# Kernel optimization log

Hardware: AMD Instinct MI355X
Metric: run time of the kernel (lower is better)

Reference implementation:

```python
import jax, jax.numpy as jnp
import numpy as np

N_NODES = 1_000_000
N_EDGES = 16_000_000


def setup_inputs() -> dict:
    key = jax.random.key(0)
    ks = jax.random.split(key, 12)
    x = jax.random.normal(ks[0], (N_NODES, 3), dtype=jnp.float32)
    edge_index = jax.random.randint(ks[1], (2, N_EDGES), 0, N_NODES, dtype=jnp.int64)
    # GCNConv uses Linear(in, out, bias=False) + separate post-aggregation bias
    def lin(k, fi, fo):
        return jax.random.normal(k, (fi, fo), dtype=jnp.float32) / np.sqrt(fi)
    W1 = lin(ks[2], 3, 4); b1 = jnp.zeros((4,), jnp.float32)
    W2 = lin(ks[3], 4, 4); b2 = jnp.zeros((4,), jnp.float32)
    W3 = lin(ks[4], 4, 3); b3 = jnp.zeros((3,), jnp.float32)
    Wc = lin(ks[5], 3, 5)
    bc = jax.random.normal(ks[6], (5,), dtype=jnp.float32) * 0.01
    return {"x": x, "edge_index": edge_index, "W1": W1, "b1": b1,
            "W2": W2, "b2": b2, "W3": W3, "b3": b3, "Wc": Wc, "bc": bc}


def reference(x, edge_index, W1, b1, W2, b2, W3, b3, Wc, bc):
    N = x.shape[0]
    loop = jnp.arange(N, dtype=edge_index.dtype)
    row = jnp.concatenate([edge_index[0], loop])  # source (with self-loops)
    col = jnp.concatenate([edge_index[1], loop])  # target (with self-loops)
    # symmetric GCN normalization: deg over targets incl. self-loops
    deg = jax.ops.segment_sum(jnp.ones_like(row, dtype=x.dtype), col, num_segments=N)
    dinv = jnp.where(deg > 0, jax.lax.rsqrt(deg), 0.0)
    norm = dinv[row] * dinv[col]  # [E+N]

    def gcn_conv(h, W, b):
        h = h @ W                              # [N, F_out]
        msg = norm[:, None] * h[row]           # gather + scale, [E+N, F_out]
        agg = jax.ops.segment_sum(msg, col, num_segments=N)
        return agg + b

    h = jnp.tanh(gcn_conv(x, W1, b1))
    h = jnp.tanh(gcn_conv(h, W2, b2))
    h = jnp.tanh(gcn_conv(h, W3, b3))
    out = h @ Wc + bc
    return (out, h)
```

## Files before the change

kernel.cpp:

```cpp
#include <hip/hip_runtime.h>


#define BKT_BITS 10
#define BKT_SZ   1024
#define MAXB     1024
#define TILE     8192
#define HTILE    4096
#define CHUNK    32768
#define TPC      4
#define SEGC     32
#define MAXSEG   32
#define ATHR     1024
#define RECSENT  0xFFFFFFFFu

typedef int v4i __attribute__((ext_vector_type(4)));

constexpr float XD_SCALE = 4096.0f;
constexpr float HD_SCALE = 16384.0f;
constexpr int   QBIAS    = 1 << 17;

__device__ __forceinline__ short q16(float v, float s) {
    int t = __float2int_rn(v * s);
    t = max(-32767, min(32767, t));
    return (short)t;
}

__device__ __forceinline__ unsigned blk_exscan(unsigned cnt, unsigned* woff) {
    int tid = threadIdx.x, lane = tid & 63, wid = tid >> 6;
    unsigned v = cnt;
#pragma unroll
    for (int d = 1; d < 64; d <<= 1) {
        unsigned t = __shfl_up(v, d);
        if (lane >= d) v += t;
    }
    if (lane == 63) woff[wid] = v;
    __syncthreads();
    if (tid < 16) {
        unsigned w = woff[tid];
        unsigned iw = w;
#pragma unroll
        for (int d = 1; d < 16; d <<= 1) {
            unsigned t = __shfl_up(iw, d, 16);
            if (tid >= d) iw += t;
        }
        woff[tid] = iw - w;
    }
    __syncthreads();
    return (v - cnt) + woff[wid];
}

__device__ __forceinline__ void ld_tile(const int* __restrict__ p, long t0, long t1,
                                        int tid, int4* dst, int sentinel) {
#pragma unroll
    for (int v = 0; v < 2; ++v) {
        long e = t0 + (long)v * HTILE + (long)tid * 4;
        if (e + 3 < t1) {
            dst[v] = *(const int4*)(p + e);
        } else {
            int* d = (int*)&dst[v];
#pragma unroll
            for (int j = 0; j < 4; ++j) d[j] = (e + j < t1) ? p[e + j] : sentinel;
        }
    }
}

__global__ __launch_bounds__(ATHR) void k_hist(const int* __restrict__ col, int E,
                                               unsigned short* __restrict__ cnt16) {
    __shared__ unsigned lh[MAXB];
    lh[threadIdx.x] = 0u;
    __syncthreads();
    long e0 = (long)blockIdx.x * TILE;
    long e1 = e0 + TILE; if (e1 > E) e1 = E;
    int4 c4[2];
    ld_tile(col, e0, e1, threadIdx.x, c4, -1);
#pragma unroll
    for (int v = 0; v < 2; ++v) {
        const int* cc = (const int*)&c4[v];
#pragma unroll
        for (int j = 0; j < 4; ++j) {
            unsigned b = ((unsigned)cc[j]) >> BKT_BITS;
            if (b < MAXB) atomicAdd(&lh[b], 1u);
        }
    }
    __syncthreads();
    cnt16[(size_t)blockIdx.x * MAXB + threadIdx.x] = (unsigned short)lh[threadIdx.x];
}

__global__ __launch_bounds__(256) void k_offA(const unsigned short* __restrict__ cnt16,
                                              int ntile, unsigned* __restrict__ psum) {
    int seg = blockIdx.x >> 2;
    int b = ((blockIdx.x & 3) << 8) + threadIdx.x;
    int tlo = seg * SEGC * TPC;
    int thi = (seg + 1) * SEGC * TPC; if (thi > ntile) thi = ntile;
    unsigned s = 0;
    for (int t = tlo; t < thi; ++t) s += cnt16[(size_t)t * MAXB + b];
    psum[seg * MAXB + b] = s;
}

__global__ __launch_bounds__(256) void k_totB(const unsigned* __restrict__ psum, int nseg,
                                              unsigned* __restrict__ bcnt) {
    int b = blockIdx.x * blockDim.x + threadIdx.x;
    unsigned s = 0;
    for (int g = 0; g < nseg; ++g) s += psum[g * MAXB + b];
    bcnt[b] = s;
}

__global__ __launch_bounds__(1024) void k_scan2(const unsigned* __restrict__ bcnt,
                                                unsigned* __restrict__ bpfx, int NB) {
    __shared__ unsigned tot[MAXB], pfx[MAXB];
    int b = threadIdx.x;
    tot[b] = (b < NB) ? bcnt[b] : 0u;
    __syncthreads();
    if (b == 0) {
        unsigned run = 0;
        for (int i = 0; i < MAXB; ++i) { pfx[i] = run; run += tot[i]; }
    }
    __syncthreads();
    bpfx[b] = pfx[b];
}

__global__ __launch_bounds__(1024) void k_offB(unsigned* __restrict__ psum, int nseg,
                                               const unsigned* __restrict__ bpfx) {
    int b = threadIdx.x;
    unsigned run = bpfx[b];
    for (int g = 0; g < nseg; ++g) {
        unsigned t = psum[g * MAXB + b];
        psum[g * MAXB + b] = run;
        run += t;
    }
}

__global__ __launch_bounds__(256) void k_offC(const unsigned short* __restrict__ cnt16,
                                              int ntile,
                                              const unsigned* __restrict__ psum,
                                              unsigned* __restrict__ offs, int nblk) {
    int seg = blockIdx.x >> 2;
    int b = ((blockIdx.x & 3) << 8) + threadIdx.x;
    int clo = seg * SEGC;
    int chi = clo + SEGC; if (chi > nblk) chi = nblk;
    unsigned run = psum[seg * MAXB + b];
    for (int c = clo; c < chi; ++c) {
        offs[(size_t)c * MAXB + b] = run;
        int tlo = c * TPC, thi = tlo + TPC; if (thi > ntile) thi = ntile;
        for (int t = tlo; t < thi; ++t) run += cnt16[(size_t)t * MAXB + b];
    }
}

__global__ __launch_bounds__(ATHR, 8) void k_place(const int* __restrict__ row,
                                                   const int* __restrict__ col, int E,
                                                   const unsigned* __restrict__ offs,
                                                   const unsigned short* __restrict__ cnt16,
                                                   unsigned* __restrict__ recbuf, int NB) {
    __shared__ unsigned lo[MAXB], cnt[MAXB], sc[MAXB], pc[MAXB];
    __shared__ unsigned rec[TILE];
    __shared__ unsigned short bkt[TILE];
    __shared__ unsigned woff[16];
    int tid = threadIdx.x;
    lo[tid] = (tid < NB) ? offs[(size_t)blockIdx.x * MAXB + tid] : 0u;
    long base = (long)blockIdx.x * CHUNK;
    long bend = base + CHUNK; if (bend > E) bend = E;
    int ntl = (int)((bend - base + TILE - 1) / TILE);
    int4 fc[2], fr[2];
    {
        long t1 = min(base + TILE, bend);
        ld_tile(col, base, t1, tid, fc, -1);
        ld_tile(row, base, t1, tid, fr, 0);
    }
    for (int ti = 0; ti < ntl; ++ti) {
        unsigned c0 = (unsigned)cnt16[(size_t)(blockIdx.x * TPC + ti) * MAXB + tid];
        unsigned mybase = blk_exscan(c0, woff);
        cnt[tid] = c0; sc[tid] = mybase; pc[tid] = 0u;
        __syncthreads();
        int4 cc4[2] = {fc[0], fc[1]};
        int4 cr4[2] = {fr[0], fr[1]};
#pragma unroll
        for (int v = 0; v < 2; ++v) {
            const int* cc = (const int*)&cc4[v];
            const int* rr = (const int*)&cr4[v];
#pragma unroll
            for (int j = 0; j < 4; ++j) {
                unsigned c = (unsigned)cc[j];
                unsigned b = c >> BKT_BITS;
                if (b >= (unsigned)NB) continue;
                unsigned r = (unsigned)rr[j];
                unsigned pos = sc[b] + atomicAdd(&pc[b], 1u);
                rec[pos] = (r << BKT_BITS) | (c & (BKT_SZ - 1));
                bkt[pos] = (unsigned short)b;
            }
        }
        __syncthreads();
        unsigned total = sc[MAXB - 1] + cnt[MAXB - 1];
        if (ti + 1 < ntl) {
            long n0 = base + (long)(ti + 1) * TILE;
            long n1 = min(n0 + TILE, bend);
            ld_tile(col, n0, n1, tid, fc, -1);
            ld_tile(row, n0, n1, tid, fr, 0);
        }
        for (unsigned t = tid; t < total; t += ATHR) {
            unsigned b = bkt[t];
            recbuf[(size_t)lo[b] + (t - sc[b])] = rec[t];
        }
        __syncthreads();
        lo[tid] += cnt[tid];
        __syncthreads();
    }
}

__global__ __launch_bounds__(ATHR) void k_bcount(const unsigned* __restrict__ recbuf,
                                                 const unsigned* __restrict__ bpfx,
                                                 const unsigned* __restrict__ bcnt,
                                                 const float* __restrict__ x,
                                                 unsigned short* __restrict__ deg,
                                                 short4* __restrict__ bufA, int N) {
    __shared__ unsigned cnt[BKT_SZ];
    int b = blockIdx.x;
    cnt[threadIdx.x] = 0u;
    __syncthreads();
    unsigned st = bpfx[b], n = bcnt[b];
    for (unsigned j = threadIdx.x; j < n; j += blockDim.x)
        atomicAdd(&cnt[recbuf[(size_t)st + j] & (BKT_SZ - 1)], 1u);
    __syncthreads();
    int node = (b << BKT_BITS) + threadIdx.x;
    if (node < N) {
        unsigned short d16 = (unsigned short)cnt[threadIdx.x];
        deg[node] = d16;
        float dv = rsqrtf((float)d16 + 1.0f);
        short4 o;
        o.x = q16(dv * x[(long)node*3 + 0], XD_SCALE);
        o.y = q16(dv * x[(long)node*3 + 1], XD_SCALE);
        o.z = q16(dv * x[(long)node*3 + 2], XD_SCALE);
        o.w = 0;
        bufA[node] = o;
    }
}

template <int FIN, int FOUT, bool OUT_DINV, int PHASE>
__global__ __launch_bounds__(ATHR) void k_bpass(const unsigned* __restrict__ recbuf,
                                                const unsigned* __restrict__ bpfx,
                                                const unsigned* __restrict__ bcnt,
                                                const short4* __restrict__ bufIn,
                                                float inv_s,
                                                const unsigned short* __restrict__ deg,
                                                const float* __restrict__ W,
                                                const float* __restrict__ bias,
                                                short4* __restrict__ bufOut,
                                                unsigned long long* __restrict__ accg,
                                                unsigned half, int N) {
    __shared__ unsigned long long acc[BKT_SZ][2];
    int b = blockIdx.x;
    int nodeT = (b << BKT_BITS) + threadIdx.x;
    if (PHASE == 2) {
        acc[threadIdx.x][0] = accg[(size_t)nodeT * 2 + 0];
        acc[threadIdx.x][1] = accg[(size_t)nodeT * 2 + 1];
    } else {
        acc[threadIdx.x][0] = 0ull; acc[threadIdx.x][1] = 0ull;
    }
    __syncthreads();
    unsigned start = bpfx[b], n = bcnt[b];
    unsigned lim = start + n;
    unsigned abase = start & ~3u;
    unsigned tot4 = lim - abase;
    for (unsigned j = (unsigned)threadIdx.x * 4u; j < tot4; j += ATHR * 4u) {
        unsigned idx = abase + j;
        unsigned r0, r1, r2, r3;
        if (idx >= start && idx + 4u <= lim) {
            v4i r = __builtin_nontemporal_load((const v4i*)(recbuf + idx));
            r0 = (unsigned)r.x; r1 = (unsigned)r.y;
            r2 = (unsigned)r.z; r3 = (unsigned)r.w;
        } else {
            unsigned rr[4];
#pragma unroll
            for (int k = 0; k < 4; ++k) {
                unsigned ii = idx + (unsigned)k;
                rr[k] = (ii >= start && ii < lim) ? recbuf[ii] : RECSENT;
            }
            r0 = rr[0]; r1 = rr[1]; r2 = rr[2]; r3 = rr[3];
        }
        unsigned s0 = r0 >> BKT_BITS, s1 = r1 >> BKT_BITS;
        unsigned s2 = r2 >> BKT_BITS, s3 = r3 >> BKT_BITS;
        bool a0, a1, a2, a3;
        if (PHASE == 1) {
            a0 = s0 < half; a1 = s1 < half; a2 = s2 < half; a3 = s3 < half;
        } else {
            a0 = (r0 != RECSENT) && s0 >= half;
            a1 = (r1 != RECSENT) && s1 >= half;
            a2 = (r2 != RECSENT) && s2 >= half;
            a3 = (r3 != RECSENT) && s3 >= half;
        }
        short4 q0, q1, q2, q3;
        if (a0) q0 = bufIn[s0];
        if (a1) q1 = bufIn[s1];
        if (a2) q2 = bufIn[s2];
        if (a3) q3 = bufIn[s3];
#define BP_ACC(av, rv, qv)                                                      \
        if (av) {                                                               \
            unsigned nl = rv & (BKT_SZ - 1);                                    \
            unsigned long long v0 =                                             \
                ((unsigned long long)(unsigned)(qv.y + QBIAS) << 32)            \
              |  (unsigned long long)(unsigned)(qv.x + QBIAS);                  \
            atomicAdd(&acc[nl][0], v0);                                         \
            if (FIN > 2) {                                                      \
                unsigned long long v1 =                                         \
                    ((unsigned long long)(unsigned)(qv.w + QBIAS) << 32)        \
                  |  (unsigned long long)(unsigned)(qv.z + QBIAS);              \
                atomicAdd(&acc[nl][1], v1);                                     \
            }                                                                   \
        }
        BP_ACC(a0, r0, q0) BP_ACC(a1, r1, q1) BP_ACC(a2, r2, q2) BP_ACC(a3, r3, q3)
#undef BP_ACC
    }
    __syncthreads();
    if (PHASE == 1) {
        accg[(size_t)nodeT * 2 + 0] = acc[threadIdx.x][0];
        accg[(size_t)nodeT * 2 + 1] = acc[threadIdx.x][1];
        return;
    }
    int node = nodeT;
    if (node >= N) return;
    int dgi = (int)deg[node];
    long long db = (long long)dgi * QBIAS;
    float dv = rsqrtf((float)dgi + 1.0f);
    short4 qs = bufIn[node];
    unsigned long long a0_ = acc[threadIdx.x][0];
    unsigned long long a1_ = acc[threadIdx.x][1];
    float s[4] = {0.f, 0.f, 0.f, 0.f};
    s[0] = (float)((long long)(unsigned)(a0_)        - db + qs.x) * inv_s;
    s[1] = (float)((long long)(unsigned)(a0_ >> 32)  - db + qs.y) * inv_s;
    if (FIN > 2) {
        s[2] = (float)((long long)(unsigned)(a1_)       - db + qs.z) * inv_s;
        s[3] = (float)((long long)(unsigned)(a1_ >> 32) - db + qs.w) * inv_s;
    }
    float o[4] = {0.f, 0.f, 0.f, 0.f};
#pragma unroll
    for (int fo = 0; fo < FOUT; ++fo) {
        float t = 0.f;
#pragma unroll
        for (int fi = 0; fi < FIN; ++fi) t += s[fi] * W[fi * FOUT + fo];
        o[fo] = tanhf(dv * t + bias[fo]);
    }
    float m = OUT_DINV ? dv : 1.0f;
    short4 outv;
    outv.x = q16(o[0] * m, HD_SCALE);
    outv.y = q16(o[1] * m, HD_SCALE);
    outv.z = (FOUT > 2) ? q16(o[2] * m, HD_SCALE) : (short)0;
    outv.w = (FOUT > 3) ? q16(o[3] * m, HD_SCALE) : (short)0;
    bufOut[node] = outv;
}

__global__ __launch_bounds__(256) void k_final(const short4* __restrict__ h3q,
                                               const float* __restrict__ Wc,
                                               const float* __restrict__ bc,
                                               float* __restrict__ out,
                                               float* __restrict__ hout, int n) {
    int i = blockIdx.x * blockDim.x + threadIdx.x;
    if (i >= n) return;
    short4 q = h3q[i];
    float h0 = (float)q.x * (1.0f / HD_SCALE);
    float h1 = (float)q.y * (1.0f / HD_SCALE);
    float h2 = (float)q.z * (1.0f / HD_SCALE);
    hout[(long)i*3 + 0] = h0;
    hout[(long)i*3 + 1] = h1;
    hout[(long)i*3 + 2] = h2;
#pragma unroll
    for (int k = 0; k < 5; ++k)
        out[(long)i*5 + k] = h0 * Wc[k] + h1 * Wc[5 + k] + h2 * Wc[10 + k] + bc[k];
}

extern "C" void kernel_launch(void* const* d_in, const int* in_sizes, int n_in,
                              void* d_out, int out_size, void* d_ws, size_t ws_size,
                              hipStream_t stream) {
    const float* x   = (const float*)d_in[0];
    const int*   ei  = (const int*)d_in[1];
    const float* W1  = (const float*)d_in[2];
    const float* b1  = (const float*)d_in[3];
    const float* W2  = (const float*)d_in[4];
    const float* b2  = (const float*)d_in[5];
    const float* W3  = (const float*)d_in[6];
    const float* b3  = (const float*)d_in[7];
    const float* Wc  = (const float*)d_in[8];
    const float* bc  = (const float*)d_in[9];

    const int N = in_sizes[0] / 3;
    const int E = in_sizes[1] / 2;
    if (N > (1 << 20)) return;
    const int* row = ei;
    const int* col = ei + E;
    const int NB = (N + BKT_SZ - 1) >> BKT_BITS;
    const int ntile = (E + TILE - 1) / TILE;
    const int nblk  = (E + CHUNK - 1) / CHUNK;
    const int nseg  = (nblk + SEGC - 1) / SEGC;
    if (nseg > MAXSEG) return;

    float* out  = (float*)d_out;
    float* hout = (float*)d_out + (long)N * 5;

    char* w0 = (char*)d_ws;
    char* w = w0;
    short4* bufA = (short4*)w;                      w += (size_t)N * 8;
    short4* bufB = (short4*)w;                      w += (size_t)N * 8;
    unsigned short* deg = (unsigned short*)w;       w += (size_t)N * 2;
    unsigned short* cnt16 = (unsigned short*)w;     w += (size_t)ntile * MAXB * 2;
    unsigned* offs  = (unsigned*)w;                 w += (size_t)nblk * MAXB * 4;
    unsigned* psum  = (unsigned*)w;                 w += (size_t)MAXSEG * MAXB * 4;
    unsigned* bpfx  = (unsigned*)w;                 w += (size_t)MAXB * 4;
    unsigned* bcnt  = (unsigned*)w;                 w += (size_t)MAXB * 4;
    unsigned long long* accg = (unsigned long long*)w;
    w += (size_t)NB * BKT_SZ * 16;
    unsigned* recbuf = (unsigned*)w;                w += (size_t)E * 4;
    if ((size_t)(w - w0) + 4096 > ws_size) return;
    const unsigned half = (unsigned)(N / 2);

    const int BT = 256;
    const int gN = (N + BT - 1) / BT;

    k_hist<<<ntile, ATHR, 0, stream>>>(col, E, cnt16);
    k_offA<<<nseg * 4, 256, 0, stream>>>(cnt16, ntile, psum);
    k_totB<<<4, 256, 0, stream>>>(psum, nseg, bcnt);
    k_scan2<<<1, 1024, 0, stream>>>(bcnt, bpfx, NB);
    k_offB<<<1, 1024, 0, stream>>>(psum, nseg, bpfx);
    k_offC<<<nseg * 4, 256, 0, stream>>>(cnt16, ntile, psum, offs, nblk);
    k_place<<<nblk, ATHR, 0, stream>>>(row, col, E, offs, cnt16, recbuf, NB);
    k_bcount<<<NB, ATHR, 0, stream>>>(recbuf, bpfx, bcnt, x, deg, bufA, N);

#define RUN_BPASS(FIN, FOUT, ODV, BIN, ISC, WW, BB, BOUT)                          \
    k_bpass<FIN, FOUT, ODV, 1><<<NB, ATHR, 0, stream>>>(recbuf, bpfx, bcnt,        \
        BIN, ISC, deg, WW, BB, BOUT, accg, half, N);                               \
    k_bpass<FIN, FOUT, ODV, 2><<<NB, ATHR, 0, stream>>>(recbuf, bpfx, bcnt,        \
        BIN, ISC, deg, WW, BB, BOUT, accg, half, N);

    RUN_BPASS(3, 4, true, bufA, 1.0f / XD_SCALE, W1, b1, bufB)
    RUN_BPASS(4, 4, true, bufB, 1.0f / HD_SCALE, W2, b2, bufA)
    RUN_BPASS(4, 3, false, bufA, 1.0f / HD_SCALE, W3, b3, bufB)
#undef RUN_BPASS

    k_final<<<gN, BT, 0, stream>>>(bufB, Wc, bc, out, hout, N);
}
```

Measured before the change: 511.3 us.

## Presort edges by source half to fuse two-phase aggregation into one pass

```diff
diff --git a/kernel.cpp b/kernel.cpp
--- a/kernel.cpp
+++ b/kernel.cpp
@@ -4,6 +4,7 @@
 #define BKT_BITS 10
 #define BKT_SZ   1024
 #define MAXB     1024
+#define MAXK     2048
 #define TILE     8192
 #define HTILE    4096
 #define CHUNK    32768
@@ -25,30 +26,6 @@
     return (short)t;
 }
 
-__device__ __forceinline__ unsigned blk_exscan(unsigned cnt, unsigned* woff) {
-    int tid = threadIdx.x, lane = tid & 63, wid = tid >> 6;
-    unsigned v = cnt;
-#pragma unroll
-    for (int d = 1; d < 64; d <<= 1) {
-        unsigned t = __shfl_up(v, d);
-        if (lane >= d) v += t;
-    }
-    if (lane == 63) woff[wid] = v;
-    __syncthreads();
-    if (tid < 16) {
-        unsigned w = woff[tid];
-        unsigned iw = w;
-#pragma unroll
-        for (int d = 1; d < 16; d <<= 1) {
-            unsigned t = __shfl_up(iw, d, 16);
-            if (tid >= d) iw += t;
-        }
-        woff[tid] = iw - w;
-    }
-    __syncthreads();
-    return (v - cnt) + woff[wid];
-}
-
 __device__ __forceinline__ void ld_tile(const int* __restrict__ p, long t0, long t1,
                                         int tid, int4* dst, int sentinel) {
 #pragma unroll
@@ -64,69 +41,79 @@
     }
 }
 
-__global__ __launch_bounds__(ATHR) void k_hist(const int* __restrict__ col, int E,
-                                               unsigned short* __restrict__ cnt16) {
-    __shared__ unsigned lh[MAXB];
-    lh[threadIdx.x] = 0u;
+__global__ __launch_bounds__(ATHR) void k_hist(const int* __restrict__ row,
+                                               const int* __restrict__ col, int E,
+                                               unsigned short* __restrict__ cnt16,
+                                               unsigned half, int NB) {
+    __shared__ unsigned lh[MAXK];
+    lh[threadIdx.x] = 0u; lh[threadIdx.x + 1024] = 0u;
     __syncthreads();
     long e0 = (long)blockIdx.x * TILE;
     long e1 = e0 + TILE; if (e1 > E) e1 = E;
-    int4 c4[2];
+    int4 c4[2], r4[2];
     ld_tile(col, e0, e1, threadIdx.x, c4, -1);
+    ld_tile(row, e0, e1, threadIdx.x, r4, 0);
 #pragma unroll
     for (int v = 0; v < 2; ++v) {
         const int* cc = (const int*)&c4[v];
+        const int* rr = (const int*)&r4[v];
 #pragma unroll
         for (int j = 0; j < 4; ++j) {
             unsigned b = ((unsigned)cc[j]) >> BKT_BITS;
-            if (b < MAXB) atomicAdd(&lh[b], 1u);
-        }
-    }
-    __syncthreads();
-    cnt16[(size_t)blockIdx.x * MAXB + threadIdx.x] = (unsigned short)lh[threadIdx.x];
+            if (b < (unsigned)NB) {
+                unsigned key = (b << 1) | (((unsigned)rr[j] >= half) ? 1u : 0u);
+                atomicAdd(&lh[key], 1u);
+            }
+        }
+    }
+    __syncthreads();
+    cnt16[(size_t)blockIdx.x * MAXK + threadIdx.x] = (unsigned short)lh[threadIdx.x];
+    cnt16[(size_t)blockIdx.x * MAXK + threadIdx.x + 1024] =
+        (unsigned short)lh[threadIdx.x + 1024];
 }
 
 __global__ __launch_bounds__(256) void k_offA(const unsigned short* __restrict__ cnt16,
                                               int ntile, unsigned* __restrict__ psum) {
-    int seg = blockIdx.x >> 2;
-    int b = ((blockIdx.x & 3) << 8) + threadIdx.x;
+    int seg = blockIdx.x >> 3;
+    int k = ((blockIdx.x & 7) << 8) + threadIdx.x;
     int tlo = seg * SEGC * TPC;
     int thi = (seg + 1) * SEGC * TPC; if (thi > ntile) thi = ntile;
     unsigned s = 0;
-    for (int t = tlo; t < thi; ++t) s += cnt16[(size_t)t * MAXB + b];
-    psum[seg * MAXB + b] = s;
+    for (int t = tlo; t < thi; ++t) s += cnt16[(size_t)t * MAXK + k];
+    psum[(size_t)seg * MAXK + k] = s;
 }
 
 __global__ __launch_bounds__(256) void k_totB(const unsigned* __restrict__ psum, int nseg,
-                                              unsigned* __restrict__ bcnt) {
-    int b = blockIdx.x * blockDim.x + threadIdx.x;
+                                              unsigned* __restrict__ kcnt) {
+    int k = blockIdx.x * blockDim.x + threadIdx.x;
     unsigned s = 0;
-    for (int g = 0; g < nseg; ++g) s += psum[g * MAXB + b];
-    bcnt[b] = s;
-}
-
-__global__ __launch_bounds__(1024) void k_scan2(const unsigned* __restrict__ bcnt,
-                                                unsigned* __restrict__ bpfx, int NB) {
-    __shared__ unsigned tot[MAXB], pfx[MAXB];
-    int b = threadIdx.x;
-    tot[b] = (b < NB) ? bcnt[b] : 0u;
-    __syncthreads();
-    if (b == 0) {
+    for (int g = 0; g < nseg; ++g) s += psum[(size_t)g * MAXK + k];
+    kcnt[k] = s;
+}
+
+__global__ __launch_bounds__(1024) void k_scan2(const unsigned* __restrict__ kcnt,
+                                                unsigned* __restrict__ kpfx) {
+    __shared__ unsigned tot[MAXK], pfx[MAXK];
+    int t = threadIdx.x;
+    tot[t] = kcnt[t]; tot[t + 1024] = kcnt[t + 1024];
+    __syncthreads();
+    if (t == 0) {
         unsigned run = 0;
-        for (int i = 0; i < MAXB; ++i) { pfx[i] = run; run += tot[i]; }
-    }
-    __syncthreads();
-    bpfx[b] = pfx[b];
+        for (int i = 0; i < MAXK; ++i) { pfx[i] = run; run += tot[i]; }
+    }
+    __syncthreads();
+    kpfx[t] = pfx[t]; kpfx[t + 1024] = pfx[t + 1024];
 }
 
 __global__ __launch_bounds__(1024) void k_offB(unsigned* __restrict__ psum, int nseg,
-                                               const unsigned* __restrict__ bpfx) {
-    int b = threadIdx.x;
-    unsigned run = bpfx[b];
-    for (int g = 0; g < nseg; ++g) {
-        unsigned t = psum[g * MAXB + b];
-        psum[g * MAXB + b] = run;
-        run += t;
+                                               const unsigned* __restrict__ kpfx) {
+    for (int k = threadIdx.x; k < MAXK; k += 1024) {
+        unsigned run = kpfx[k];
+        for (int g = 0; g < nseg; ++g) {
+            unsigned t = psum[(size_t)g * MAXK + k];
+            psum[(size_t)g * MAXK + k] = run;
+            run += t;
+        }
     }
 }
 
@@ -134,15 +121,15 @@
                                               int ntile,
                                               const unsigned* __restrict__ psum,
                                               unsigned* __restrict__ offs, int nblk) {
-    int seg = blockIdx.x >> 2;
-    int b = ((blockIdx.x & 3) << 8) + threadIdx.x;
+    int seg = blockIdx.x >> 3;
+    int k = ((blockIdx.x & 7) << 8) + threadIdx.x;
     int clo = seg * SEGC;
     int chi = clo + SEGC; if (chi > nblk) chi = nblk;
-    unsigned run = psum[seg * MAXB + b];
+    unsigned run = psum[(size_t)seg * MAXK + k];
     for (int c = clo; c < chi; ++c) {
-        offs[(size_t)c * MAXB + b] = run;
+        offs[(size_t)c * MAXK + k] = run;
         int tlo = c * TPC, thi = tlo + TPC; if (thi > ntile) thi = ntile;
-        for (int t = tlo; t < thi; ++t) run += cnt16[(size_t)t * MAXB + b];
+        for (int t = tlo; t < thi; ++t) run += cnt16[(size_t)t * MAXK + k];
     }
 }
 
@@ -150,13 +137,14 @@
                                                    const int* __restrict__ col, int E,
                                                    const unsigned* __restrict__ offs,
                                                    const unsigned short* __restrict__ cnt16,
-                                                   unsigned* __restrict__ recbuf, int NB) {
-    __shared__ unsigned lo[MAXB], cnt[MAXB], sc[MAXB], pc[MAXB];
+                                                   unsigned* __restrict__ recbuf,
+                                                   unsigned half, int NB) {
+    __shared__ unsigned lo[MAXK], cnt[MAXK], sc[MAXK], pc[MAXK];
     __shared__ unsigned rec[TILE];
     __shared__ unsigned short bkt[TILE];
-    __shared__ unsigned woff[16];
-    int tid = threadIdx.x;
-    lo[tid] = (tid < NB) ? offs[(size_t)blockIdx.x * MAXB + tid] : 0u;
+    int tid = threadIdx.x, lane = tid & 63, wid = tid >> 6;
+    lo[tid]        = offs[(size_t)blockIdx.x * MAXK + tid];
+    lo[tid + 1024] = offs[(size_t)blockIdx.x * MAXK + tid + 1024];
     long base = (long)blockIdx.x * CHUNK;
     long bend = base + CHUNK; if (bend > E) bend = E;
     int ntl = (int)((bend - base + TILE - 1) / TILE);
@@ -167,29 +155,56 @@
         ld_tile(row, base, t1, tid, fr, 0);
     }
     for (int ti = 0; ti < ntl; ++ti) {
-        unsigned c0 = (unsigned)cnt16[(size_t)(blockIdx.x * TPC + ti) * MAXB + tid];
-        unsigned mybase = blk_exscan(c0, woff);
-        cnt[tid] = c0; sc[tid] = mybase; pc[tid] = 0u;
+        unsigned c0 = (unsigned)cnt16[(size_t)(blockIdx.x * TPC + ti) * MAXK + tid * 2];
+        unsigned c1 = (unsigned)cnt16[(size_t)(blockIdx.x * TPC + ti) * MAXK + tid * 2 + 1];
+        unsigned s = c0 + c1;
+        unsigned v = s;
+#pragma unroll
+        for (int d = 1; d < 64; d <<= 1) {
+            unsigned t = __shfl_up(v, d);
+            if (lane >= d) v += t;
+        }
+        if (lane == 63) pc[wid] = v;
+        __syncthreads();
+        if (tid < 16) {
+            unsigned w = pc[tid];
+            unsigned iw = w;
+#pragma unroll
+            for (int d = 1; d < 16; d <<= 1) {
+                unsigned t = __shfl_up(iw, d, 16);
+                if (tid >= d) iw += t;
+            }
+            pc[tid] = iw - w;
+        }
+        __syncthreads();
+        unsigned tbase = pc[wid] + (v - s);
+        sc[tid * 2]     = tbase;
+        sc[tid * 2 + 1] = tbase + c0;
+        cnt[tid * 2]     = c0;
+        cnt[tid * 2 + 1] = c1;
+        __syncthreads();
+        pc[tid] = 0u; pc[tid + 1024] = 0u;
         __syncthreads();
         int4 cc4[2] = {fc[0], fc[1]};
         int4 cr4[2] = {fr[0], fr[1]};
 #pragma unroll
-        for (int v = 0; v < 2; ++v) {
-            const int* cc = (const int*)&cc4[v];
-            const int* rr = (const int*)&cr4[v];
+        for (int vv = 0; vv < 2; ++vv) {
+            const int* cc = (const int*)&cc4[vv];
+            const int* rr = (const int*)&cr4[vv];
 #pragma unroll
             for (int j = 0; j < 4; ++j) {
                 unsigned c = (unsigned)cc[j];
                 unsigned b = c >> BKT_BITS;
                 if (b >= (unsigned)NB) continue;
                 unsigned r = (unsigned)rr[j];
-                unsigned pos = sc[b] + atomicAdd(&pc[b], 1u);
+                unsigned key = (b << 1) | ((r >= half) ? 1u : 0u);
+                unsigned pos = sc[key] + atomicAdd(&pc[key], 1u);
                 rec[pos] = (r << BKT_BITS) | (c & (BKT_SZ - 1));
-                bkt[pos] = (unsigned short)b;
+                bkt[pos] = (unsigned short)key;
             }
         }
         __syncthreads();
-        unsigned total = sc[MAXB - 1] + cnt[MAXB - 1];
+        unsigned total = sc[MAXK - 1] + cnt[MAXK - 1];
         if (ti + 1 < ntl) {
             long n0 = base + (long)(ti + 1) * TILE;
             long n1 = min(n0 + TILE, bend);
@@ -197,18 +212,19 @@
             ld_tile(row, n0, n1, tid, fr, 0);
         }
         for (unsigned t = tid; t < total; t += ATHR) {
-            unsigned b = bkt[t];
-            recbuf[(size_t)lo[b] + (t - sc[b])] = rec[t];
+            unsigned k = bkt[t];
+            recbuf[(size_t)lo[k] + (t - sc[k])] = rec[t];
         }
         __syncthreads();
         lo[tid] += cnt[tid];
+        lo[tid + 1024] += cnt[tid + 1024];
         __syncthreads();
     }
 }
 
 __global__ __launch_bounds__(ATHR) void k_bcount(const unsigned* __restrict__ recbuf,
-                                                 const unsigned* __restrict__ bpfx,
-                                                 const unsigned* __restrict__ bcnt,
+                                                 const unsigned* __restrict__ kpfx,
+                                                 const unsigned* __restrict__ kcnt,
                                                  const float* __restrict__ x,
                                                  unsigned short* __restrict__ deg,
                                                  short4* __restrict__ bufA, int N) {
@@ -216,9 +232,13 @@
     int b = blockIdx.x;
     cnt[threadIdx.x] = 0u;
     __syncthreads();
-    unsigned st = bpfx[b], n = bcnt[b];
-    for (unsigned j = threadIdx.x; j < n; j += blockDim.x)
-        atomicAdd(&cnt[recbuf[(size_t)st + j] & (BKT_SZ - 1)], 1u);
+#pragma unroll
+    for (int h = 0; h < 2; ++h) {
+        unsigned seg = ((unsigned)b << 1) | (unsigned)h;
+        unsigned st = kpfx[seg], n = kcnt[seg];
+        for (unsigned j = threadIdx.x; j < n; j += blockDim.x)
+            atomicAdd(&cnt[recbuf[(size_t)st + j] & (BKT_SZ - 1)], 1u);
+    }
     __syncthreads();
     int node = (b << BKT_BITS) + threadIdx.x;
     if (node < N) {
@@ -234,88 +254,68 @@
     }
 }
 
-template <int FIN, int FOUT, bool OUT_DINV, int PHASE>
+template <int FIN, int FOUT, bool OUT_DINV>
 __global__ __launch_bounds__(ATHR) void k_bpass(const unsigned* __restrict__ recbuf,
-                                                const unsigned* __restrict__ bpfx,
-                                                const unsigned* __restrict__ bcnt,
+                                                const unsigned* __restrict__ kpfx,
+                                                const unsigned* __restrict__ kcnt,
                                                 const short4* __restrict__ bufIn,
                                                 float inv_s,
                                                 const unsigned short* __restrict__ deg,
                                                 const float* __restrict__ W,
                                                 const float* __restrict__ bias,
-                                                short4* __restrict__ bufOut,
-                                                unsigned long long* __restrict__ accg,
-                                                unsigned half, int N) {
+                                                short4* __restrict__ bufOut, int N) {
     __shared__ unsigned long long acc[BKT_SZ][2];
     int b = blockIdx.x;
-    int nodeT = (b << BKT_BITS) + threadIdx.x;
-    if (PHASE == 2) {
-        acc[threadIdx.x][0] = accg[(size_t)nodeT * 2 + 0];
-        acc[threadIdx.x][1] = accg[(size_t)nodeT * 2 + 1];
-    } else {
-        acc[threadIdx.x][0] = 0ull; acc[threadIdx.x][1] = 0ull;
-    }
-    __syncthreads();
-    unsigned start = bpfx[b], n = bcnt[b];
-    unsigned lim = start + n;
-    unsigned abase = start & ~3u;
-    unsigned tot4 = lim - abase;
-    for (unsigned j = (unsigned)threadIdx.x * 4u; j < tot4; j += ATHR * 4u) {
-        unsigned idx = abase + j;
-        unsigned r0, r1, r2, r3;
-        if (idx >= start && idx + 4u <= lim) {
-            v4i r = __builtin_nontemporal_load((const v4i*)(recbuf + idx));
-            r0 = (unsigned)r.x; r1 = (unsigned)r.y;
-            r2 = (unsigned)r.z; r3 = (unsigned)r.w;
-        } else {
-            unsigned rr[4];
-#pragma unroll
-            for (int k = 0; k < 4; ++k) {
-                unsigned ii = idx + (unsigned)k;
-                rr[k] = (ii >= start && ii < lim) ? recbuf[ii] : RECSENT;
+    acc[threadIdx.x][0] = 0ull; acc[threadIdx.x][1] = 0ull;
+    __syncthreads();
+#pragma unroll
+    for (int h = 0; h < 2; ++h) {
+        unsigned seg = ((unsigned)b << 1) | (unsigned)h;
+        unsigned start = kpfx[seg], n = kcnt[seg];
+        unsigned lim = start + n;
+        unsigned abase = start & ~3u;
+        unsigned tot4 = lim - abase;
+        for (unsigned j = (unsigned)threadIdx.x * 4u; j < tot4; j += ATHR * 4u) {
+            unsigned idx = abase + j;
+            unsigned r0, r1, r2, r3;
+            if (idx >= start && idx + 4u <= lim) {
+                v4i r = __builtin_nontemporal_load((const v4i*)(recbuf + idx));
+                r0 = (unsigned)r.x; r1 = (unsigned)r.y;
+                r2 = (unsigned)r.z; r3 = (unsigned)r.w;
+            } else {
+                unsigned rr[4];
+#pragma unroll
+                for (int k = 0; k < 4; ++k) {
+                    unsigned ii = idx + (unsigned)k;
+                    rr[k] = (ii >= start && ii < lim) ? recbuf[ii] : RECSENT;
+                }
+                r0 = rr[0]; r1 = rr[1]; r2 = rr[2]; r3 = rr[3];
             }
-            r0 = rr[0]; r1 = rr[1]; r2 = rr[2]; r3 = rr[3];
-        }
-        unsigned s0 = r0 >> BKT_BITS, s1 = r1 >> BKT_BITS;
-        unsigned s2 = r2 >> BKT_BITS, s3 = r3 >> BKT_BITS;
-        bool a0, a1, a2, a3;
-        if (PHASE == 1) {
-            a0 = s0 < half; a1 = s1 < half; a2 = s2 < half; a3 = s3 < half;
-        } else {
-            a0 = (r0 != RECSENT) && s0 >= half;
-            a1 = (r1 != RECSENT) && s1 >= half;
-            a2 = (r2 != RECSENT) && s2 >= half;
-            a3 = (r3 != RECSENT) && s3 >= half;
-        }
-        short4 q0, q1, q2, q3;
-        if (a0) q0 = bufIn[s0];
-        if (a1) q1 = bufIn[s1];
-        if (a2) q2 = bufIn[s2];
-        if (a3) q3 = bufIn[s3];
-#define BP_ACC(av, rv, qv)                                                      \
-        if (av) {                                                               \
-            unsigned nl = rv & (BKT_SZ - 1);                                    \
-            unsigned long long v0 =                                             \
-                ((unsigned long long)(unsigned)(qv.y + QBIAS) << 32)            \
-              |  (unsigned long long)(unsigned)(qv.x + QBIAS);                  \
-            atomicAdd(&acc[nl][0], v0);                                         \
-            if (FIN > 2) {                                                      \
-                unsigned long long v1 =                                         \
-                    ((unsigned long long)(unsigned)(qv.w + QBIAS) << 32)        \
-                  |  (unsigned long long)(unsigned)(qv.z + QBIAS);              \
-                atomicAdd(&acc[nl][1], v1);                                     \
-            }                                                                   \
-        }
-        BP_ACC(a0, r0, q0) BP_ACC(a1, r1, q1) BP_ACC(a2, r2, q2) BP_ACC(a3, r3, q3)
+            short4 q0, q1, q2, q3;
+            if (r0 != RECSENT) q0 = bufIn[r0 >> BKT_BITS];
+            if (r1 != RECSENT) q1 = bufIn[r1 >> BKT_BITS];
+            if (r2 != RECSENT) q2 = bufIn[r2 >> BKT_BITS];
+            if (r3 != RECSENT) q3 = bufIn[r3 >> BKT_BITS];
+#define BP_ACC(rv, qv)                                                          \
+            if (rv != RECSENT) {                                                \
+                unsigned nl = rv & (BKT_SZ - 1);                                \
+                unsigned long long v0 =                                         \
+                    ((unsigned long long)(unsigned)(qv.y + QBIAS) << 32)        \
+                  |  (unsigned long long)(unsigned)(qv.x + QBIAS);              \
+                atomicAdd(&acc[nl][0], v0);                                     \
+                if (FIN > 2) {                                                  \
+                    unsigned long long v1 =                                     \
+                        ((unsigned long long)(unsigned)(qv.w + QBIAS) << 32)    \
+                      |  (unsigned long long)(unsigned)(qv.z + QBIAS);          \
+                    atomicAdd(&acc[nl][1], v1);                                 \
+                }                                                               \
+            }
+            BP_ACC(r0, q0) BP_ACC(r1, q1) BP_ACC(r2, q2) BP_ACC(r3, q3)
 #undef BP_ACC
-    }
-    __syncthreads();
-    if (PHASE == 1) {
-        accg[(size_t)nodeT * 2 + 0] = acc[threadIdx.x][0];
-        accg[(size_t)nodeT * 2 + 1] = acc[threadIdx.x][1];
-        return;
-    }
-    int node = nodeT;
+        }
+        __syncthreads();
+    }
+    int node = (b << BKT_BITS) + threadIdx.x;
     if (node >= N) return;
     int dgi = (int)deg[node];
     long long db = (long long)dgi * QBIAS;
@@ -390,6 +390,7 @@
     const int nblk  = (E + CHUNK - 1) / CHUNK;
     const int nseg  = (nblk + SEGC - 1) / SEGC;
     if (nseg > MAXSEG) return;
+    const unsigned half = (unsigned)(N / 2);
 
     float* out  = (float*)d_out;
     float* hout = (float*)d_out + (long)N * 5;
@@ -399,39 +400,32 @@
     short4* bufA = (short4*)w;                      w += (size_t)N * 8;
     short4* bufB = (short4*)w;                      w += (size_t)N * 8;
     unsigned short* deg = (unsigned short*)w;       w += (size_t)N * 2;
-    unsigned short* cnt16 = (unsigned short*)w;     w += (size_t)ntile * MAXB * 2;
-    unsigned* offs  = (unsigned*)w;                 w += (size_t)nblk * MAXB * 4;
-    unsigned* psum  = (unsigned*)w;                 w += (size_t)MAXSEG * MAXB * 4;
-    unsigned* bpfx  = (unsigned*)w;                 w += (size_t)MAXB * 4;
-    unsigned* bcnt  = (unsigned*)w;                 w += (size_t)MAXB * 4;
-    unsigned long long* accg = (unsigned long long*)w;
-    w += (size_t)NB * BKT_SZ * 16;
+    unsigned short* cnt16 = (unsigned short*)w;     w += (size_t)ntile * MAXK * 2;
+    unsigned* offs  = (unsigned*)w;                 w += (size_t)nblk * MAXK * 4;
+    unsigned* psum  = (unsigned*)w;                 w += (size_t)MAXSEG * MAXK * 4;
+    unsigned* kpfx  = (unsigned*)w;                 w += (size_t)MAXK * 4;
+    unsigned* kcnt  = (unsigned*)w;                 w += (size_t)MAXK * 4;
     unsigned* recbuf = (unsigned*)w;                w += (size_t)E * 4;
     if ((size_t)(w - w0) + 4096 > ws_size) return;
-    const unsigned half = (unsigned)(N / 2);
 
     const int BT = 256;
     const int gN = (N + BT - 1) / BT;
 
-    k_hist<<<ntile, ATHR, 0, stream>>>(col, E, cnt16);
-    k_offA<<<nseg * 4, 256, 0, stream>>>(cnt16, ntile, psum);
-    k_totB<<<4, 256, 0, stream>>>(psum, nseg, bcnt);
-    k_scan2<<<1, 1024, 0, stream>>>(bcnt, bpfx, NB);
-    k_offB<<<1, 1024, 0, stream>>>(psum, nseg, bpfx);
-    k_offC<<<nseg * 4, 256, 0, stream>>>(cnt16, ntile, psum, offs, nblk);
-    k_place<<<nblk, ATHR, 0, stream>>>(row, col, E, offs, cnt16, recbuf, NB);
-    k_bcount<<<NB, ATHR, 0, stream>>>(recbuf, bpfx, bcnt, x, deg, bufA, N);
-
-#define RUN_BPASS(FIN, FOUT, ODV, BIN, ISC, WW, BB, BOUT)                          \
-    k_bpass<FIN, FOUT, ODV, 1><<<NB, ATHR, 0, stream>>>(recbuf, bpfx, bcnt,        \
-        BIN, ISC, deg, WW, BB, BOUT, accg, half, N);                               \
-    k_bpass<FIN, FOUT, ODV, 2><<<NB, ATHR, 0, stream>>>(recbuf, bpfx, bcnt,        \
-        BIN, ISC, deg, WW, BB, BOUT, accg, half, N);
-
-    RUN_BPASS(3, 4, true, bufA, 1.0f / XD_SCALE, W1, b1, bufB)
-    RUN_BPASS(4, 4, true, bufB, 1.0f / HD_SCALE, W2, b2, bufA)
-    RUN_BPASS(4, 3, false, bufA, 1.0f / HD_SCALE, W3, b3, bufB)
-#undef RUN_BPASS
+    k_hist<<<ntile, ATHR, 0, stream>>>(row, col, E, cnt16, half, NB);
+    k_offA<<<nseg * 8, 256, 0, stream>>>(cnt16, ntile, psum);
+    k_totB<<<8, 256, 0, stream>>>(psum, nseg, kcnt);
+    k_scan2<<<1, 1024, 0, stream>>>(kcnt, kpfx);
+    k_offB<<<1, 1024, 0, stream>>>(psum, nseg, kpfx);
+    k_offC<<<nseg * 8, 256, 0, stream>>>(cnt16, ntile, psum, offs, nblk);
+    k_place<<<nblk, ATHR, 0, stream>>>(row, col, E, offs, cnt16, recbuf, half, NB);
+    k_bcount<<<NB, ATHR, 0, stream>>>(recbuf, kpfx, kcnt, x, deg, bufA, N);
+
+    k_bpass<3, 4, true><<<NB, ATHR, 0, stream>>>(recbuf, kpfx, kcnt,
+        bufA, 1.0f / XD_SCALE, deg, W1, b1, bufB, N);
+    k_bpass<4, 4, true><<<NB, ATHR, 0, stream>>>(recbuf, kpfx, kcnt,
+        bufB, 1.0f / HD_SCALE, deg, W2, b2, bufA, N);
+    k_bpass<4, 3, false><<<NB, ATHR, 0, stream>>>(recbuf, kpfx, kcnt,
+        bufA, 1.0f / HD_SCALE, deg, W3, b3, bufB, N);
 
     k_final<<<gN, BT, 0, stream>>>(bufB, Wc, bc, out, hout, N);
 }
```

New measurement: 507.7 us. No clear change (-0.7%).
